# Kernel optimization log

Measured on AMD Instinct MI355X. Metric: run time of the kernel, lower is better.

Reference implementation:

```python
import jax, jax.numpy as jnp
import numpy as np

ETA = 3.0       # eta_px
KCAP = 96       # k_pos_cap
POS_W = 1.2     # obj_pos_weight
LCD = 1.0       # lambda_cd
LP0 = 1.0       # lambda_p0


def setup_inputs() -> dict:
    key = jax.random.key(0)
    k1, k2, k3, k4, k5, k6 = jax.random.split(key, 6)
    B, H, W, Ng, C = 4, 192, 192, 64, 4
    img = 192 * 8.0
    ctr = jax.random.uniform(k4, (B, Ng, 1, 2), minval=60.0, maxval=img - 60.0)
    offs = jax.random.normal(k5, (B, Ng, 3, 2)) * 30.0
    return {
        "pred_reg": jax.random.normal(k1, (B, 6, H, W), dtype=jnp.float32),
        "pred_obj": jax.random.normal(k2, (B, 1, H, W), dtype=jnp.float32),
        "pred_cls": jax.random.normal(k3, (B, C, H, W), dtype=jnp.float32),
        "gt_pts": (ctr + offs).astype(jnp.float32),
        "gt_lbl": jax.random.randint(k6, (B, Ng), 0, C),
        "stride": 8,
    }


def _loss_core(pred_reg, pred_obj, pred_cls, gt_pts, gt_lbl, stride):
    B, _, H, W = pred_reg.shape
    N = H * W
    C = pred_cls.shape[1]
    s = jnp.float32(stride)
    ys = (jnp.arange(H, dtype=jnp.float32) + 0.5) * s
    xs = (jnp.arange(W, dtype=jnp.float32) + 0.5) * s
    yy, xx = jnp.meshgrid(ys, xs, indexing='ij')
    px = xx.reshape(N)  # grid-center x, [N]
    py = yy.reshape(N)

    A = gt_pts[:, :, 0, :]   # [B,Ng,2]
    Bv = gt_pts[:, :, 1, :]
    Cv = gt_pts[:, :, 2, :]

    def sgn(P, Q):  # sign test of cell center vs edge (P,Q); broadcasts to [B,Ng,N]
        return (px - Q[..., 0:1]) * (P[..., 1:2] - Q[..., 1:2]) - (P[..., 0:1] - Q[..., 0:1]) * (py - Q[..., 1:2])

    d1 = sgn(A, Bv); d2 = sgn(Bv, Cv); d3 = sgn(Cv, A)
    has_neg = (d1 < 0) | (d2 < 0) | (d3 < 0)
    has_pos = (d1 > 0) | (d2 > 0) | (d3 > 0)
    inside = ~(has_neg & has_pos)  # [B,Ng,N]

    def seg(P, Q):  # point-to-segment distance, [B,Ng,N]
        vx = Q[..., 0:1] - P[..., 0:1]
        vy = Q[..., 1:2] - P[..., 1:2]
        wx = px - P[..., 0:1]
        wy = py - P[..., 1:2]
        t = jnp.clip((wx * vx + wy * vy) / (vx * vx + vy * vy + 1e-9), 0.0, 1.0)
        dx = wx - t * vx
        dy = wy - t * vy
        return jnp.sqrt(dx * dx + dy * dy + 1e-12)

    dist = jnp.minimum(seg(A, Bv), jnp.minimum(seg(Bv, Cv), seg(Cv, A)))  # [B,Ng,N]
    pos = inside | (dist <= ETA)

    # top-k cap: keep the KCAP closest positive cells per GT (matches torch topk(-d))
    dmask = jnp.where(pos, dist, jnp.inf)
    negv, idx = jax.lax.top_k(-dmask, KCAP)  # [B,Ng,KCAP]
    valid = jnp.isfinite(negv)               # True only for actual positives
    capped = jax.vmap(jax.vmap(lambda i, v: jnp.zeros((N,), bool).at[i].set(v)))(idx, valid)  # [B,Ng,N]

    # objectness BCE-with-logits with pos_weight, summed
    obj_t = capped.any(axis=1).astype(pred_obj.dtype)  # [B,N]
    x = pred_obj.reshape(B, N)
    obj_loss = jnp.sum(-(POS_W * obj_t * jax.nn.log_sigmoid(x) + (1.0 - obj_t) * jax.nn.log_sigmoid(-x)))

    # class targets: nearest GT (by triangle distance) among capped positives
    dcls = jnp.where(capped, dist, jnp.inf)
    jbest = jnp.argmin(dcls, axis=1)                   # [B,N]; first index on ties, like sequential strict <
    cellmask = jnp.isfinite(jnp.min(dcls, axis=1))     # [B,N]
    tgt = jnp.take_along_axis(gt_lbl, jbest, axis=1)   # [B,N]
    logits = pred_cls.reshape(B, C, N).transpose(0, 2, 1)  # [B,N,C]
    lse = jax.nn.logsumexp(logits, axis=-1)
    picked = jnp.take_along_axis(logits, tgt[..., None], axis=-1)[..., 0]
    cls_loss = jnp.sum(jnp.where(cellmask, lse - picked, 0.0))

    centers_flat = jnp.stack([px, py], axis=-1)        # [N,2]
    anchors = centers_flat[idx]                        # [B,Ng,K,2]
    pred_off = pred_reg.transpose(0, 2, 3, 1).reshape(B, N, 3, 2)
    pred_sel = jax.vmap(lambda p, i: p[i])(pred_off, idx)          # [B,Ng,K,3,2]
    gt_off = (gt_pts[:, :, None, :, :] - anchors[:, :, :, None, :]) / s  # [B,Ng,K,3,2]
    w = valid.astype(pred_reg.dtype)                   # [B,Ng,K]

    loss_p0 = jnp.sum(w * jnp.sum((pred_sel[..., 0, :] - gt_off[..., 0, :]) ** 2, axis=-1))
    # chamfer between the 2 tail points; original: chamfer_2pts(...) * npix == per-cell (d1+d2) summed
    dmat = jnp.sqrt(jnp.sum((pred_sel[:, :, :, 1:, None, :] - gt_off[:, :, :, None, 1:, :]) ** 2, axis=-1) + 1e-12)  # [B,Ng,K,2,2]
    cd = jnp.sum(w * (dmat.min(axis=-1).sum(axis=-1) + dmat.min(axis=-2).sum(axis=-1)))
    reg_loss = LP0 * loss_p0 + LCD * cd

    return jnp.stack([reg_loss, obj_loss, cls_loss])


def reference(pred_reg, pred_obj, pred_cls, gt_pts, gt_lbl, stride):
    return _loss_core(pred_reg, pred_obj, pred_cls, gt_pts, gt_lbl, stride)
```

## Files before the change

### kernel.cpp

```cpp
#include <hip/hip_runtime.h>
#include <stdint.h>

#define ETA    3.0f
#define KCAP   96
#define POS_W  1.2f
#define NG     64
#define BATCH  4
#define HH     192
#define WW     192
#define NCELL  (HH*WW)
#define NCLS   4
#define CAP    4096
#define PTHR   256
#define NWAVE  4
#define NBLK   (BATCH*NG)
#define SEGS   16
#define NB2    (BATCH*SEGS)
#define SEGC   (NCELL/SEGS)
#define BCLAIM (NG*KCAP)
#define INF64  0xFFFFFFFFFFFFFFFFull
#define TOPBIT 0x8000000000000000ull

#define WS_CCNT  16
#define WS_CLAIM (WS_CCNT + NBLK*4)
#define WS_PA    (WS_CLAIM + NBLK*KCAP*8)
#define WS_PC    (WS_PA + NBLK*8)

#define OBJ4_PER_BLK 144

__device__ __forceinline__ float log_sigmoid(float x) {
    return fminf(x, 0.0f) - __logf(1.0f + __expf(-fabsf(x)));
}

__device__ __forceinline__ float segsq(float wx, float wy, float vx, float vy, float inv) {
    float t = (wx * vx + wy * vy) * inv;
    t = fminf(fmaxf(t, 0.0f), 1.0f);
    float dx = wx - t * vx;
    float dy = wy - t * vy;
    return dx * dx + dy * dy;
}

template <int NQ>
__device__ __forceinline__ void block_red(float v[NQ], float* sbuf) {
    #pragma unroll
    for (int off = 32; off > 0; off >>= 1) {
        #pragma unroll
        for (int q = 0; q < NQ; ++q) v[q] += __shfl_down(v[q], off);
    }
    const int lane = threadIdx.x & 63;
    const int wid  = threadIdx.x >> 6;
    __syncthreads();
    if (lane == 0) {
        #pragma unroll
        for (int q = 0; q < NQ; ++q) sbuf[wid * NQ + q] = v[q];
    }
    __syncthreads();
    if (threadIdx.x == 0) {
        #pragma unroll
        for (int q = 0; q < NQ; ++q) {
            float r = 0.0f;
            #pragma unroll
            for (int w = 0; w < NWAVE; ++w) r += sbuf[w * NQ + q];
            v[q] = r;
        }
    }
}

__global__ __launch_bounds__(PTHR)
void pair_kernel(const float* __restrict__ pred_reg,
                 const float* __restrict__ pred_obj,
                 const float* __restrict__ gt_pts,
                 const int*   __restrict__ stride_p,
                 unsigned* __restrict__ ccnt,
                 unsigned long long* __restrict__ claims,
                 float2* __restrict__ pA,
                 int* __restrict__ arrival)
{
    const int pair = blockIdx.x;
    const int b    = pair >> 6;
    const int tid  = threadIdx.x;
    const int lane = tid & 63;
    const int wid  = tid >> 6;
    const float s  = (float)(*stride_p);

    __shared__ unsigned long long keys[CAP];
    __shared__ int   hist[PTHR];
    __shared__ float sbuf[NWAVE * 5];
    __shared__ int   wsum[NWAVE];
    __shared__ int   scnt, ccl, sd, sp;

    if (pair == 0 && tid == 0) *arrival = 0;

    float c_obj = 0.0f;
    if (tid < OBJ4_PER_BLK) {
        const float4 v = ((const float4*)pred_obj)[pair * OBJ4_PER_BLK + tid];
        c_obj = -log_sigmoid(-v.x) - log_sigmoid(-v.y)
                - log_sigmoid(-v.z) - log_sigmoid(-v.w);
    }

    const float* gp = gt_pts + (size_t)pair * 6;
    const float Ax = gp[0], Ay = gp[1];
    const float Bx = gp[2], By = gp[3];
    const float Cx = gp[4], Cy = gp[5];

    const float vABx = Bx - Ax, vABy = By - Ay;
    const float vBCx = Cx - Bx, vBCy = Cy - By;
    const float vCAx = Ax - Cx, vCAy = Ay - Cy;
    const float invAB = 1.0f / (vABx * vABx + vABy * vABy + 1e-9f);
    const float invBC = 1.0f / (vBCx * vBCx + vBCy * vBCy + 1e-9f);
    const float invCA = 1.0f / (vCAx * vCAx + vCAy * vCAy + 1e-9f);

    const float xmin = fminf(Ax, fminf(Bx, Cx)) - ETA;
    const float xmax = fmaxf(Ax, fmaxf(Bx, Cx)) + ETA;
    const float ymin = fminf(Ay, fminf(By, Cy)) - ETA;
    const float ymax = fmaxf(Ay, fmaxf(By, Cy)) + ETA;
    const float inv_sf = 1.0f / s;
    int j0 = max(0,      (int)floorf(xmin * inv_sf - 0.5f) - 1);
    int j1 = min(WW - 1, (int)ceilf (xmax * inv_sf - 0.5f) + 1);
    int i0 = max(0,      (int)floorf(ymin * inv_sf - 0.5f) - 1);
    int i1 = min(HH - 1, (int)ceilf (ymax * inv_sf - 0.5f) + 1);
    const int nbw = j1 - j0 + 1;
    const int nbh = i1 - i0 + 1;
    const int nb  = (nbw > 0 && nbh > 0) ? nbw * nbh : 0;

    if (tid == 0) { scnt = 0; ccl = 0; }
    __syncthreads();

    for (int t = tid; t < nb; t += PTHR) {
        const int li = t / nbw;
        const int lj = t - li * nbw;
        const int i = i0 + li;
        const int j = j0 + lj;
        const float px = ((float)j + 0.5f) * s;
        const float py = ((float)i + 0.5f) * s;

        const float d1 = (px - Bx) * (Ay - By) - (Ax - Bx) * (py - By);
        const float d2 = (px - Cx) * (By - Cy) - (Bx - Cx) * (py - Cy);
        const float d3 = (px - Ax) * (Cy - Ay) - (Cx - Ax) * (py - Ay);
        const bool has_neg = (d1 < 0.0f) | (d2 < 0.0f) | (d3 < 0.0f);
        const bool has_pos = (d1 > 0.0f) | (d2 > 0.0f) | (d3 > 0.0f);
        const bool inside = !(has_neg && has_pos);

        float dsq = segsq(px - Ax, py - Ay, vABx, vABy, invAB);
        dsq = fminf(dsq, segsq(px - Bx, py - By, vBCx, vBCy, invBC));
        dsq = fminf(dsq, segsq(px - Cx, py - Cy, vCAx, vCAy, invCA));
        const float dist = sqrtf(dsq + 1e-12f);

        if (inside || dist <= ETA) {
            int slot = atomicAdd(&scnt, 1);
            if (slot < CAP) {
                const int n = i * WW + j;
                keys[slot] = (((unsigned long long)__float_as_uint(dist)) << 16) | (unsigned)n;
            }
        }
    }
    __syncthreads();

    const int M = min(scnt, CAP);
    unsigned long long T = INF64;

    if (M > KCAP) {
        unsigned long long prefix = 0;
        int need = KCAP;
        for (int shift = 40; shift >= 0; shift -= 8) {
            hist[tid] = 0;
            __syncthreads();
            for (int t = tid; t < M; t += PTHR) {
                const unsigned long long k = keys[t];
                if ((k >> (shift + 8)) == prefix)
                    atomicAdd(&hist[(int)((k >> shift) & 0xFF)], 1);
            }
            __syncthreads();
            const int h = hist[tid];
            int incl = h;
            #pragma unroll
            for (int off = 1; off < 64; off <<= 1) {
                const int o = __shfl_up(incl, off);
                if (lane >= off) incl += o;
            }
            if (lane == 63) wsum[wid] = incl;
            __syncthreads();
            #pragma unroll
            for (int w = 0; w < NWAVE; ++w) if (w < wid) incl += wsum[w];
            const int excl = incl - h;
            if (excl < need && incl >= need) { sd = tid; sp = excl; }
            __syncthreads();
            prefix = (prefix << 8) | (unsigned)sd;
            need  -= sp;
            __syncthreads();
        }
        T = prefix;
    }

    float c_reg = 0.0f;
    for (int t = tid; t < M; t += PTHR) {
        const unsigned long long k = keys[t];
        if (k > T) continue;
        const int n = (int)(k & 0xFFFFull);

        const int slot = atomicAdd(&ccl, 1);
        if (slot < KCAP)
            claims[(size_t)pair * KCAP + slot] =
                ((k >> 16) << 32) | (unsigned long long)(unsigned)n;

        const int i = n / WW;
        const int j = n - i * WW;
        const float ax = ((float)j + 0.5f) * s;
        const float ay = ((float)i + 0.5f) * s;

        const float g0x = (Ax - ax) * inv_sf, g0y = (Ay - ay) * inv_sf;
        const float g1x = (Bx - ax) * inv_sf, g1y = (By - ay) * inv_sf;
        const float g2x = (Cx - ax) * inv_sf, g2y = (Cy - ay) * inv_sf;

        const float* pr = pred_reg + (size_t)b * 6 * NCELL + n;
        const float p0x = pr[0 * NCELL], p0y = pr[1 * NCELL];
        const float p1x = pr[2 * NCELL], p1y = pr[3 * NCELL];
        const float p2x = pr[4 * NCELL], p2y = pr[5 * NCELL];

        c_reg += (p0x - g0x) * (p0x - g0x) + (p0y - g0y) * (p0y - g0y);

        const float d11 = sqrtf((p1x - g1x) * (p1x - g1x) + (p1y - g1y) * (p1y - g1y) + 1e-12f);
        const float d12 = sqrtf((p1x - g2x) * (p1x - g2x) + (p1y - g2y) * (p1y - g2y) + 1e-12f);
        const float d21 = sqrtf((p2x - g1x) * (p2x - g1x) + (p2y - g1y) * (p2y - g1y) + 1e-12f);
        const float d22 = sqrtf((p2x - g2x) * (p2x - g2x) + (p2y - g2y) * (p2y - g2y) + 1e-12f);

        c_reg += fminf(d11, d12) + fminf(d21, d22)
               + fminf(d11, d21) + fminf(d12, d22);
    }
    __syncthreads();
    if (tid == 0) ccnt[pair] = (unsigned)min(ccl, KCAP);

    float v[2] = { c_reg, c_obj };
    block_red<2>(v, sbuf);
    if (tid == 0) pA[pair] = make_float2(v[0], v[1]);
}

__global__ __launch_bounds__(PTHR)
void resolve_kernel(const float* __restrict__ pred_obj,
                    const float* __restrict__ pred_cls,
                    const int*   __restrict__ gt_lbl,
                    const unsigned* __restrict__ ccnt,
                    const unsigned long long* __restrict__ claims,
                    const float2* __restrict__ pA,
                    float4* __restrict__ pC,
                    int* __restrict__ arrival,
                    float* __restrict__ out)
{
    const int blk = blockIdx.x;
    const int b   = blk >> 4;
    const int seg = blk & (SEGS - 1);
    const int n0  = seg * SEGC;
    const int tid = threadIdx.x;

    __shared__ unsigned long long cl[BCLAIM];
    __shared__ unsigned table[SEGC];
    __shared__ int   cnts[NG];
    __shared__ float sbuf[NWAVE * 5];
    __shared__ int   ccl, islast;

    if (tid < NG) cnts[tid] = (int)ccnt[b * NG + tid];
    if (tid == 0) { ccl = 0; islast = 0; }
    for (int i = tid; i < SEGC; i += PTHR) table[i] = 0xFFFFFFFFu;
    __syncthreads();

    const unsigned long long* bcl = claims + (size_t)b * BCLAIM;
    #pragma unroll 1
    for (int q = tid; q < BCLAIM / 2; q += PTHR) {
        const int sIdx = 2 * q;
        const int pg = sIdx / KCAP;
        const int r  = sIdx - pg * KCAP;
        const int cnt = cnts[pg];
        if (r >= cnt) continue;
        const ulonglong2 e2 = ((const ulonglong2*)bcl)[q];
        {
            const unsigned long long e = e2.x;
            const int ln = (int)(e & 0xFFFFull) - n0;
            if ((unsigned)ln < (unsigned)SEGC) {
                const int i = atomicAdd(&ccl, 1);
                cl[i] = e | ((unsigned long long)pg << 16);
                atomicMin(&table[ln], (unsigned)(e >> 32));
            }
        }
        if (r + 1 < cnt) {
            const unsigned long long e = e2.y;
            const int ln = (int)(e & 0xFFFFull) - n0;
            if ((unsigned)ln < (unsigned)SEGC) {
                const int i = atomicAdd(&ccl, 1);
                cl[i] = e | ((unsigned long long)pg << 16);
                atomicMin(&table[ln], (unsigned)(e >> 32));
            }
        }
    }
    __syncthreads();
    const int NC = ccl;

    for (int i = tid; i < NC; i += PTHR) {
        const unsigned long long e = cl[i];
        const int ln = (int)(e & 0xFFFFull) - n0;
        if (table[ln] == (unsigned)(e >> 32)) cl[i] = e | TOPBIT;
    }
    __syncthreads();
    for (int i = tid; i < NC; i += PTHR) {
        const unsigned long long e = cl[i];
        if (e & TOPBIT) {
            const int ln = (int)(e & 0xFFFFull) - n0;
            atomicMin(&table[ln], (unsigned)((e >> 16) & 63ull));
        }
    }
    __syncthreads();

    float v[3] = { 0.0f, 0.0f, 0.0f };
    const size_t bc = (size_t)b * NCLS * NCELL;
    for (int i = tid; i < NC; i += PTHR) {
        const unsigned long long e = cl[i];
        if (!(e & TOPBIT)) continue;
        const int n = (int)(e & 0xFFFFull);
        const int g = (int)((e >> 16) & 63ull);
        if (table[n - n0] != (unsigned)g) continue;

        const float x = pred_obj[b * NCELL + n];
        v[0] += (-POS_W * log_sigmoid(x)) + log_sigmoid(-x);

        const float* pc = pred_cls + bc + n;
        const float l0 = pc[0];
        const float l1 = pc[NCELL];
        const float l2 = pc[2 * NCELL];
        const float l3 = pc[3 * NCELL];
        const float m = fmaxf(fmaxf(l0, l1), fmaxf(l2, l3));
        v[1] += m + __logf(__expf(l0 - m) + __expf(l1 - m)
                         + __expf(l2 - m) + __expf(l3 - m));
        const int tgt = gt_lbl[b * NG + g];
        v[2] += (tgt == 0) ? l0 : (tgt == 1) ? l1 : (tgt == 2) ? l2 : l3;
    }
    block_red<3>(v, sbuf);

    if (tid == 0) {
        pC[blk] = make_float4(v[0], v[1], v[2], 0.0f);
        __threadfence();
        const int old = atomicAdd(arrival, 1);
        if (old == NB2 - 1) islast = 1;
    }
    __syncthreads();
    if (!islast) return;
    __threadfence();

    const float2 a = pA[tid];
    const float4 c = (tid < NB2) ? pC[tid] : make_float4(0.f, 0.f, 0.f, 0.f);
    float w[5] = { a.x, a.y, c.x, c.y, c.z };
    block_red<5>(w, sbuf);
    if (tid == 0) {
        out[0] = w[0];
        out[1] = w[1] + w[2];
        out[2] = w[3] - w[4];
    }
}

extern "C" void kernel_launch(void* const* d_in, const int* in_sizes, int n_in,
                              void* d_out, int out_size, void* d_ws, size_t ws_size,
                              hipStream_t stream) {
    const float* pred_reg = (const float*)d_in[0];
    const float* pred_obj = (const float*)d_in[1];
    const float* pred_cls = (const float*)d_in[2];
    const float* gt_pts   = (const float*)d_in[3];
    const int*   gt_lbl   = (const int*)d_in[4];
    const int*   stride_p = (const int*)d_in[5];
    float* out = (float*)d_out;

    char* ws = (char*)d_ws;
    int*      arrival = (int*)ws;
    unsigned* ccnt    = (unsigned*)(ws + WS_CCNT);
    unsigned long long* claims = (unsigned long long*)(ws + WS_CLAIM);
    float2*   pA      = (float2*)(ws + WS_PA);
    float4*   pC      = (float4*)(ws + WS_PC);

    (void)in_sizes; (void)n_in; (void)ws_size; (void)out_size;

    hipLaunchKernelGGL(pair_kernel, dim3(NBLK), dim3(PTHR), 0, stream,
                       pred_reg, pred_obj, gt_pts, stride_p,
                       ccnt, claims, pA, arrival);
    hipLaunchKernelGGL(resolve_kernel, dim3(NB2), dim3(PTHR), 0, stream,
                       pred_obj, pred_cls, gt_lbl, ccnt, claims, pA,
                       pC, arrival, out);
}
```

Before: 20.56 us.

## Pack claim key with GT index in 64-bit atomicMin and widen resolve blocks

The resolve kernel now packs the claim distance key and GT index into one 64-bit value and resolves ownership with a single atomicMin pass. This removes two extra passes over the claim list and their barriers. The resolve kernel also runs 1024 threads per block instead of 256, and the radix-select in the pair kernel exits early once the selected bucket exactly fills the remaining count. The trade-offs are 64-bit LDS atomics, a doubled-size table, and more waves taking part in each block reduction.

```diff
diff --git a/kernel.cpp b/kernel.cpp
--- a/kernel.cpp
+++ b/kernel.cpp
@@ -13,13 +13,14 @@
 #define CAP    4096
 #define PTHR   256
 #define NWAVE  4
+#define PTHR2  1024
+#define NWAVE2 (PTHR2/64)
 #define NBLK   (BATCH*NG)
 #define SEGS   16
 #define NB2    (BATCH*SEGS)
 #define SEGC   (NCELL/SEGS)
 #define BCLAIM (NG*KCAP)
 #define INF64  0xFFFFFFFFFFFFFFFFull
-#define TOPBIT 0x8000000000000000ull
 
 #define WS_CCNT  16
 #define WS_CLAIM (WS_CCNT + NBLK*4)
@@ -40,7 +41,7 @@
     return dx * dx + dy * dy;
 }
 
-template <int NQ>
+template <int NQ, int NW>
 __device__ __forceinline__ void block_red(float v[NQ], float* sbuf) {
     #pragma unroll
     for (int off = 32; off > 0; off >>= 1) {
@@ -60,7 +61,7 @@
         for (int q = 0; q < NQ; ++q) {
             float r = 0.0f;
             #pragma unroll
-            for (int w = 0; w < NWAVE; ++w) r += sbuf[w * NQ + q];
+            for (int w = 0; w < NW; ++w) r += sbuf[w * NQ + q];
             v[q] = r;
         }
     }
@@ -85,7 +86,7 @@
 
     __shared__ unsigned long long keys[CAP];
     __shared__ int   hist[PTHR];
-    __shared__ float sbuf[NWAVE * 5];
+    __shared__ float sbuf[NWAVE * 2];
     __shared__ int   wsum[NWAVE];
     __shared__ int   scnt, ccl, sd, sp;
 
@@ -187,9 +188,15 @@
             __syncthreads();
             prefix = (prefix << 8) | (unsigned)sd;
             need  -= sp;
-            __syncthreads();
-        }
-        T = prefix;
+            const int hsel = hist[sd];
+            __syncthreads();
+            if (hsel == need) {
+                T = (shift == 0) ? prefix
+                                 : ((prefix << shift) | ((1ull << shift) - 1ull));
+                break;
+            }
+            if (shift == 0) T = prefix;
+        }
     }
 
     float c_reg = 0.0f;
@@ -231,11 +238,11 @@
     if (tid == 0) ccnt[pair] = (unsigned)min(ccl, KCAP);
 
     float v[2] = { c_reg, c_obj };
-    block_red<2>(v, sbuf);
+    block_red<2, NWAVE>(v, sbuf);
     if (tid == 0) pA[pair] = make_float2(v[0], v[1]);
 }
 
-__global__ __launch_bounds__(PTHR)
+__global__ __launch_bounds__(PTHR2)
 void resolve_kernel(const float* __restrict__ pred_obj,
                     const float* __restrict__ pred_cls,
                     const int*   __restrict__ gt_lbl,
@@ -253,19 +260,19 @@
     const int tid = threadIdx.x;
 
     __shared__ unsigned long long cl[BCLAIM];
-    __shared__ unsigned table[SEGC];
+    __shared__ unsigned long long table[SEGC];
     __shared__ int   cnts[NG];
-    __shared__ float sbuf[NWAVE * 5];
+    __shared__ float sbuf[NWAVE2 * 5];
     __shared__ int   ccl, islast;
 
     if (tid < NG) cnts[tid] = (int)ccnt[b * NG + tid];
     if (tid == 0) { ccl = 0; islast = 0; }
-    for (int i = tid; i < SEGC; i += PTHR) table[i] = 0xFFFFFFFFu;
+    for (int i = tid; i < SEGC; i += PTHR2) table[i] = INF64;
     __syncthreads();
 
     const unsigned long long* bcl = claims + (size_t)b * BCLAIM;
     #pragma unroll 1
-    for (int q = tid; q < BCLAIM / 2; q += PTHR) {
+    for (int q = tid; q < BCLAIM / 2; q += PTHR2) {
         const int sIdx = 2 * q;
         const int pg = sIdx / KCAP;
         const int r  = sIdx - pg * KCAP;
@@ -278,7 +285,8 @@
             if ((unsigned)ln < (unsigned)SEGC) {
                 const int i = atomicAdd(&ccl, 1);
                 cl[i] = e | ((unsigned long long)pg << 16);
-                atomicMin(&table[ln], (unsigned)(e >> 32));
+                atomicMin(&table[ln],
+                          (e & 0xFFFFFFFF00000000ull) | (unsigned long long)pg);
             }
         }
         if (r + 1 < cnt) {
@@ -287,36 +295,23 @@
             if ((unsigned)ln < (unsigned)SEGC) {
                 const int i = atomicAdd(&ccl, 1);
                 cl[i] = e | ((unsigned long long)pg << 16);
-                atomicMin(&table[ln], (unsigned)(e >> 32));
+                atomicMin(&table[ln],
+                          (e & 0xFFFFFFFF00000000ull) | (unsigned long long)pg);
             }
         }
     }
     __syncthreads();
     const int NC = ccl;
-
-    for (int i = tid; i < NC; i += PTHR) {
-        const unsigned long long e = cl[i];
-        const int ln = (int)(e & 0xFFFFull) - n0;
-        if (table[ln] == (unsigned)(e >> 32)) cl[i] = e | TOPBIT;
-    }
-    __syncthreads();
-    for (int i = tid; i < NC; i += PTHR) {
-        const unsigned long long e = cl[i];
-        if (e & TOPBIT) {
-            const int ln = (int)(e & 0xFFFFull) - n0;
-            atomicMin(&table[ln], (unsigned)((e >> 16) & 63ull));
-        }
-    }
-    __syncthreads();
 
     float v[3] = { 0.0f, 0.0f, 0.0f };
     const size_t bc = (size_t)b * NCLS * NCELL;
-    for (int i = tid; i < NC; i += PTHR) {
+    for (int i = tid; i < NC; i += PTHR2) {
         const unsigned long long e = cl[i];
-        if (!(e & TOPBIT)) continue;
         const int n = (int)(e & 0xFFFFull);
         const int g = (int)((e >> 16) & 63ull);
-        if (table[n - n0] != (unsigned)g) continue;
+        if (table[n - n0] !=
+            ((e & 0xFFFFFFFF00000000ull) | (unsigned long long)(unsigned)g))
+            continue;
 
         const float x = pred_obj[b * NCELL + n];
         v[0] += (-POS_W * log_sigmoid(x)) + log_sigmoid(-x);
@@ -332,7 +327,7 @@
         const int tgt = gt_lbl[b * NG + g];
         v[2] += (tgt == 0) ? l0 : (tgt == 1) ? l1 : (tgt == 2) ? l2 : l3;
     }
-    block_red<3>(v, sbuf);
+    block_red<3, NWAVE2>(v, sbuf);
 
     if (tid == 0) {
         pC[blk] = make_float4(v[0], v[1], v[2], 0.0f);
@@ -344,10 +339,10 @@
     if (!islast) return;
     __threadfence();
 
-    const float2 a = pA[tid];
-    const float4 c = (tid < NB2) ? pC[tid] : make_float4(0.f, 0.f, 0.f, 0.f);
-    float w[5] = { a.x, a.y, c.x, c.y, c.z };
-    block_red<5>(w, sbuf);
+    float w[5] = { 0.0f, 0.0f, 0.0f, 0.0f, 0.0f };
+    if (tid < NBLK) { const float2 a = pA[tid]; w[0] = a.x; w[1] = a.y; }
+    if (tid < NB2)  { const float4 c = pC[tid]; w[2] = c.x; w[3] = c.y; w[4] = c.z; }
+    block_red<5, NWAVE2>(w, sbuf);
     if (tid == 0) {
         out[0] = w[0];
         out[1] = w[1] + w[2];
@@ -378,7 +373,7 @@
     hipLaunchKernelGGL(pair_kernel, dim3(NBLK), dim3(PTHR), 0, stream,
                        pred_reg, pred_obj, gt_pts, stride_p,
                        ccnt, claims, pA, arrival);
-    hipLaunchKernelGGL(resolve_kernel, dim3(NB2), dim3(PTHR), 0, stream,
+    hipLaunchKernelGGL(resolve_kernel, dim3(NB2), dim3(PTHR2), 0, stream,
                        pred_obj, pred_cls, gt_lbl, ccnt, claims, pA,
                        pC, arrival, out);
 }
```

Result: no change. 20.85 us (+1.4%).
